# Kernel tuning notes

Hardware: AMD Instinct MI355X
Metric: run time of the kernel (lower is better)

Reference implementation:

```python
import jax, jax.numpy as jnp
import numpy as np

B, T, D = 2, 2048, 1024
H, HD = 16, 64
MAX_LEN = 2048


def setup_inputs() -> dict:
    key = jax.random.key(0)
    ks = jax.random.split(key, 7)
    s = 0.02
    return {
        "x": jax.random.normal(ks[0], (B, T, D), dtype=jnp.float32),
        "qkv_w": jax.random.normal(ks[1], (3 * D, D), dtype=jnp.float32) * s,
        "qkv_b": jax.random.normal(ks[2], (3 * D,), dtype=jnp.float32) * s,
        "out_w": jax.random.normal(ks[3], (D, D), dtype=jnp.float32) * s,
        "out_b": jax.random.normal(ks[4], (D,), dtype=jnp.float32) * s,
        "rel_pos": jax.random.normal(ks[5], (2 * MAX_LEN - 1, HD), dtype=jnp.float32),
        "rpe_w": jax.random.normal(ks[6], (HD,), dtype=jnp.float32) * s,
    }


def reference(x, qkv_w, qkv_b, out_w, out_b, rel_pos, rpe_w):
    Bq, Tq, Dq = x.shape
    scale = HD ** -0.5
    qkv = x @ qkv_w.T + qkv_b  # [B,T,3D]
    qkv = qkv.reshape(Bq, Tq, 3, H, HD)
    q = qkv[:, :, 0].transpose(0, 2, 1, 3)  # [B,H,T,HD]
    k = qkv[:, :, 1].transpose(0, 2, 1, 3)
    v = qkv[:, :, 2].transpose(0, 2, 1, 3)
    scores = jnp.einsum('bhqd,bhkd->bhqk', q, k) * scale  # [B,H,T,T]
    # relative position bias: gather rel embeddings, project to scalar
    rel_idx = jnp.arange(Tq)[None, :] - jnp.arange(Tq)[:, None] + MAX_LEN - 1  # [T,T]
    bias = (rel_pos @ rpe_w)[rel_idx]  # project first (cheap), then gather -> [T,T]
    scores = scores + bias[None, None]
    attn = jax.nn.softmax(scores, axis=-1)
    out = jnp.einsum('bhqk,bhkd->bhqd', attn, v)  # [B,H,T,HD]
    out = out.transpose(0, 2, 1, 3).reshape(Bq, Tq, Dq)
    return out @ out_w.T + out_b
```

## Files before the change

kernel.cpp:

```cpp
#include <hip/hip_runtime.h>
#include <math.h>

#define B_ 2
#define T_ 2048
#define D_ 1024
#define H_ 16
#define HD_ 64
#define MAXLEN_ 2048
#define N3D_ 3072
#define M_ (B_ * T_)
#define KA 1024

#define SCALE_L2E 0.18033688011116215f
#define L2E 1.4426950408889634f

typedef unsigned short ushort_t;
typedef __attribute__((ext_vector_type(8))) short short8;
typedef __attribute__((ext_vector_type(4))) float floatx4;
#define MFMA16(a, b, c) __builtin_amdgcn_mfma_f32_16x16x32_bf16(a, b, c, 0, 0, 0)

static __device__ __forceinline__ ushort_t f2bf(float f) {
    unsigned u = __float_as_uint(f);
    unsigned r = (u + 0x7FFFu + ((u >> 16) & 1u)) >> 16;
    return (ushort_t)r;
}
static __device__ __forceinline__ unsigned packrnu(float a, float b) {
    unsigned ua = __float_as_uint(a) + 0x8000u;
    unsigned ub = __float_as_uint(b) + 0x8000u;
    return __builtin_amdgcn_perm(ub, ua, 0x07060302u);
}

static __device__ __forceinline__ void gld16(const ushort_t* g, ushort_t* l) {
    __builtin_amdgcn_global_load_lds(
        (const __attribute__((address_space(1))) void*)g,
        (__attribute__((address_space(3))) void*)l, 16, 0, 0);
}

__global__ __launch_bounds__(256) void cvt_all(
    const float* __restrict__ x, const float* __restrict__ qw,
    const float* __restrict__ ow, const float* __restrict__ rel_pos,
    const float* __restrict__ rpe_w,
    ushort_t* __restrict__ Xc, ushort_t* __restrict__ QWc,
    ushort_t* __restrict__ OWc, float* __restrict__ biasp)
{
    const int row = blockIdx.x;
    if (row < M_ + N3D_ + D_) {
        const float* src; ushort_t* dst; int r;
        if (row < M_)            { src = x;  dst = Xc;  r = row; }
        else if (row < M_ + N3D_){ src = qw; dst = QWc; r = row - M_; }
        else                     { src = ow; dst = OWc; r = row - M_ - N3D_; }
        const int c = threadIdx.x * 4;
        float4 v = *(const float4*)(src + (size_t)r * 1024 + c);
        ushort4 hv;
        hv.x = f2bf(v.x); hv.y = f2bf(v.y); hv.z = f2bf(v.z); hv.w = f2bf(v.w);
        *(ushort4*)(dst + (size_t)r * KA + c) = hv;
    } else {
        const int wv = threadIdx.x >> 6, lane = threadIdx.x & 63;
        const int r = (row - (M_ + N3D_ + D_)) * 4 + wv;
        if (r < 2 * MAXLEN_ - 1) {
            float v = rel_pos[(size_t)r * HD_ + lane] * rpe_w[lane];
#pragma unroll
            for (int off = 32; off; off >>= 1) v += __shfl_down(v, off);
            if (lane == 0) biasp[r] = v * L2E;
        }
    }
}

__global__ __launch_bounds__(256) void qkv_mfma(
    const ushort_t* __restrict__ Ac, const ushort_t* __restrict__ Bc,
    const float* __restrict__ bias,
    ushort_t* __restrict__ Qs, ushort_t* __restrict__ Khi,
    ushort_t* __restrict__ Vt)
{
    __shared__ __align__(16) ushort_t As[2][16 * 512];
    __shared__ __align__(16) ushort_t Bs[2][16 * 512];
    const int tid = threadIdx.x;
    const int wv = tid >> 6, lane = tid & 63;
    const int l16 = lane & 15, quad = lane >> 4;
    const int wm = wv & 1, wn = wv >> 1;

    const int orig = blockIdx.y * 24 + blockIdx.x;
    const int swz = (orig & 7) * 96 + (orig >> 3);
    const int m0 = (swz / 24) * 128, n0 = (swz % 24) * 128;

    floatx4 acc[4][4];
#pragma unroll
    for (int i = 0; i < 4; ++i)
#pragma unroll
        for (int j = 0; j < 4; ++j) acc[i][j] = (floatx4){0.f, 0.f, 0.f, 0.f};

    auto stage = [&](int bufi, int kk) {
#pragma unroll
        for (int c = 0; c < 4; ++c) {
            const int b = wv * 4 + c;
            const int i = b >> 1, ks = b & 1;
            const int k = kk + ks * 32 + quad * 8;
            gld16(Ac + (size_t)(m0 + i * 16 + l16) * KA + k, As[bufi] + b * 512);
            gld16(Bc + (size_t)(n0 + i * 16 + l16) * KA + k, Bs[bufi] + b * 512);
        }
    };

    stage(0, 0);
    __syncthreads();

#pragma unroll 1
    for (int t = 0; t < 16; ++t) {
        const int cur = t & 1;
        if (t < 15) stage(cur ^ 1, (t + 1) * 64);
#pragma unroll
        for (int ks = 0; ks < 2; ++ks) {
            short8 af[4], bf[4];
#pragma unroll
            for (int ii = 0; ii < 4; ++ii)
                af[ii] = *(const short8*)(As[cur] + ((wm * 4 + ii) * 2 + ks) * 512 + lane * 8);
#pragma unroll
            for (int jj = 0; jj < 4; ++jj)
                bf[jj] = *(const short8*)(Bs[cur] + ((wn * 4 + jj) * 2 + ks) * 512 + lane * 8);
#pragma unroll
            for (int ii = 0; ii < 4; ++ii)
#pragma unroll
                for (int jj = 0; jj < 4; ++jj)
                    acc[ii][jj] = MFMA16(af[ii], bf[jj], acc[ii][jj]);
        }
        if (t < 15) __syncthreads();
    }

#pragma unroll
    for (int ii = 0; ii < 4; ++ii) {
#pragma unroll
        for (int r = 0; r < 4; ++r) {
            const int m = m0 + wm * 64 + ii * 16 + quad * 4 + r;
            const int bb = m >> 11, t = m & 2047;
#pragma unroll
            for (int jj = 0; jj < 4; ++jj) {
                const int n = n0 + wn * 64 + jj * 16 + l16;
                const int c = n >> 10, h = (n >> 6) & 15, hd = n & 63;
                const float v = acc[ii][jj][r] + bias[n];
                const size_t idx = (((size_t)bb * H_ + h) * T_ + t) * HD_ + hd;
                if (c == 0) { Qs[idx] = f2bf(v * SCALE_L2E); }
                else if (c == 1) { Khi[idx] = f2bf(v); }
                else { Vt[(((size_t)bb * H_ + h) * HD_ + hd) * T_ + t] = f2bf(v); }
            }
        }
    }
}

__global__ __launch_bounds__(256) void out_mfma(
    const ushort_t* __restrict__ Ac, const ushort_t* __restrict__ Bc,
    const float* __restrict__ bias, float* __restrict__ Out)
{
    __shared__ __align__(16) ushort_t As[2][16 * 512];
    __shared__ __align__(16) ushort_t Bs[2][8 * 512];
    const int tid = threadIdx.x;
    const int wv = tid >> 6, lane = tid & 63;
    const int l16 = lane & 15, quad = lane >> 4;
    const int wm = wv & 1, wn = wv >> 1;

    const int orig = blockIdx.y * 16 + blockIdx.x;
    const int swz = (orig & 7) * 64 + (orig >> 3);
    const int m0 = (swz >> 4) * 128, n0 = (swz & 15) * 64;

    floatx4 acc[4][2];
#pragma unroll
    for (int i = 0; i < 4; ++i)
#pragma unroll
        for (int j = 0; j < 2; ++j) acc[i][j] = (floatx4){0.f, 0.f, 0.f, 0.f};

    auto stage = [&](int bufi, int kk) {
#pragma unroll
        for (int c = 0; c < 4; ++c) {
            const int b = wv * 4 + c;
            const int i = b >> 1, ks = b & 1;
            const int k = kk + ks * 32 + quad * 8;
            gld16(Ac + (size_t)(m0 + i * 16 + l16) * KA + k, As[bufi] + b * 512);
        }
#pragma unroll
        for (int c = 0; c < 2; ++c) {
            const int b = wv * 2 + c;
            const int j = b >> 1, ks = b & 1;
            const int k = kk + ks * 32 + quad * 8;
            gld16(Bc + (size_t)(n0 + j * 16 + l16) * KA + k, Bs[bufi] + b * 512);
        }
    };

    stage(0, 0);
    __syncthreads();

#pragma unroll 1
    for (int t = 0; t < 16; ++t) {
        const int cur = t & 1;
        if (t < 15) stage(cur ^ 1, (t + 1) * 64);
#pragma unroll
        for (int ks = 0; ks < 2; ++ks) {
            short8 af[4], bf[2];
#pragma unroll
            for (int ii = 0; ii < 4; ++ii)
                af[ii] = *(const short8*)(As[cur] + ((wm * 4 + ii) * 2 + ks) * 512 + lane * 8);
#pragma unroll
            for (int jj = 0; jj < 2; ++jj)
                bf[jj] = *(const short8*)(Bs[cur] + ((wn * 2 + jj) * 2 + ks) * 512 + lane * 8);
#pragma unroll
            for (int ii = 0; ii < 4; ++ii)
#pragma unroll
                for (int jj = 0; jj < 2; ++jj)
                    acc[ii][jj] = MFMA16(af[ii], bf[jj], acc[ii][jj]);
        }
        if (t < 15) __syncthreads();
    }

#pragma unroll
    for (int ii = 0; ii < 4; ++ii) {
#pragma unroll
        for (int r = 0; r < 4; ++r) {
            const int m = m0 + wm * 64 + ii * 16 + quad * 4 + r;
#pragma unroll
            for (int jj = 0; jj < 2; ++jj) {
                const int n = n0 + wn * 32 + jj * 16 + l16;
                Out[(size_t)m * D_ + n] = acc[ii][jj][r] + bias[n];
            }
        }
    }
}

__global__ __launch_bounds__(256) void attn_mfma(
    const ushort_t* __restrict__ Qs, const ushort_t* __restrict__ Khi,
    const ushort_t* __restrict__ Vt, const float* __restrict__ biasp,
    ushort_t* __restrict__ AOc)
{
    __shared__ __align__(16) ushort_t KS[2][8 * 512];
    __shared__ __align__(16) ushort_t VS[2][8 * 512];
    __shared__ __align__(16) ushort_t PS[4][2][1024];

    const int i = blockIdx.x;
    const int j = i >> 3;
    const int bh = (i & 7) + 8 * (j >> 4);
    const int q0 = (j & 15) * 128;
    const int tid = threadIdx.x;
    const int wv = tid >> 6, lane = tid & 63;
    const int l16 = lane & 15, quad = lane >> 4;

    const int qw = q0 + wv * 32;

    short8 qh[2][2];
#pragma unroll
    for (int u = 0; u < 2; ++u) {
        const size_t qoff = ((size_t)bh * T_ + qw + u * 16 + l16) * HD_ + quad * 8;
        qh[u][0] = *(const short8*)(Qs + qoff);
        qh[u][1] = *(const short8*)(Qs + qoff + 32);
    }

    float l_r[2] = {0.f, 0.f};
    floatx4 o_acc[4][2];
#pragma unroll
    for (int g2 = 0; g2 < 4; ++g2)
#pragma unroll
        for (int u = 0; u < 2; ++u) o_acc[g2][u] = (floatx4){0.f, 0.f, 0.f, 0.f};

    const ushort_t* gK = Khi + (size_t)bh * T_ * HD_;
    const ushort_t* gV = Vt + (size_t)bh * HD_ * T_;
    const int c0base = 2047 + quad * 4 - (qw + 16 + l16);
    const int qdbase = quad >> 1;

    const size_t kstage = (size_t)(wv * 16 + l16) * HD_ + quad * 8;
    const size_t vstage = (size_t)(wv * 16 + l16) * T_ + quad * 8;

    gld16(gK + kstage,      KS[0] + (wv * 2 + 0) * 512);
    gld16(gK + kstage + 32, KS[0] + (wv * 2 + 1) * 512);
    gld16(gV + vstage,      VS[0] + (wv * 2 + 0) * 512);
    gld16(gV + vstage + 32, VS[0] + (wv * 2 + 1) * 512);
    __syncthreads();

    for (int t = 0; t < 32; ++t) {
        const int k0 = t * 64;
        const int buf = t & 1, nbuf = buf ^ 1;

        float4 f4[5];
        {
            const float* bp = biasp + (c0base + k0);
#pragma unroll
            for (int z = 0; z < 5; ++z)
                __builtin_memcpy(&f4[z], bp + z * 16, 16);
        }

        if (t < 31) {
            const size_t koff = kstage + (size_t)(k0 + 64) * HD_;
            gld16(gK + koff,      KS[nbuf] + (wv * 2 + 0) * 512);
            gld16(gK + koff + 32, KS[nbuf] + (wv * 2 + 1) * 512);
            const size_t voff = vstage + (size_t)(k0 + 64);
            gld16(gV + voff,      VS[nbuf] + (wv * 2 + 0) * 512);
            gld16(gV + voff + 32, VS[nbuf] + (wv * 2 + 1) * 512);
        }

#pragma unroll
        for (int g = 0; g < 4; ++g) {
            const short8 kh0 = *(const short8*)(KS[buf] + (g * 2 + 0) * 512 + lane * 8);
            const short8 kh1 = *(const short8*)(KS[buf] + (g * 2 + 1) * 512 + lane * 8);
            const int qd = 2 * (g & 1) + qdbase;
#pragma unroll
            for (int u = 0; u < 2; ++u) {
                const float4 bbv = f4[g + 1 - u];
                floatx4 a = (floatx4){bbv.x, bbv.y, bbv.z, bbv.w};
                a = MFMA16(kh0, qh[u][0], a);
                a = MFMA16(kh1, qh[u][1], a);
                const float p0 = __builtin_amdgcn_exp2f(a[0]);
                const float p1 = __builtin_amdgcn_exp2f(a[1]);
                const float p2 = __builtin_amdgcn_exp2f(a[2]);
                const float p3 = __builtin_amdgcn_exp2f(a[3]);
                l_r[u] += (p0 + p1) + (p2 + p3);
                uint2 pkd;
                pkd.x = packrnu(p0, p1);
                pkd.y = packrnu(p2, p3);
                *(uint2*)(PS[wv][u] + (g >> 1) * 512 + (qd * 16 + l16) * 8 + (quad & 1) * 4) = pkd;
            }
        }

        short8 pf[2][2];
#pragma unroll
        for (int u = 0; u < 2; ++u) {
            pf[u][0] = *(const short8*)(PS[wv][u] + lane * 8);
            pf[u][1] = *(const short8*)(PS[wv][u] + 512 + lane * 8);
        }

#pragma unroll
        for (int g2 = 0; g2 < 4; ++g2) {
            const short8 v0 = *(const short8*)(VS[buf] + (g2 * 2 + 0) * 512 + lane * 8);
            const short8 v1 = *(const short8*)(VS[buf] + (g2 * 2 + 1) * 512 + lane * 8);
#pragma unroll
            for (int u = 0; u < 2; ++u) {
                o_acc[g2][u] = MFMA16(v0, pf[u][0], o_acc[g2][u]);
                o_acc[g2][u] = MFMA16(v1, pf[u][1], o_acc[g2][u]);
            }
        }
        __syncthreads();
    }

    const int bb2 = bh >> 4, h2 = bh & 15;
#pragma unroll
    for (int u = 0; u < 2; ++u) {
        l_r[u] += __shfl_xor(l_r[u], 16);
        l_r[u] += __shfl_xor(l_r[u], 32);
        const float inv = 1.0f / l_r[u];
        const size_t m = (size_t)bb2 * T_ + qw + u * 16 + l16;
#pragma unroll
        for (int g2 = 0; g2 < 4; ++g2) {
            uint2 pk;
            pk.x = packrnu(o_acc[g2][u][0] * inv, o_acc[g2][u][1] * inv);
            pk.y = packrnu(o_acc[g2][u][2] * inv, o_acc[g2][u][3] * inv);
            *(uint2*)(AOc + m * KA + h2 * 64 + g2 * 16 + quad * 4) = pk;
        }
    }
}

extern "C" void kernel_launch(void* const* d_in, const int* in_sizes, int n_in,
                              void* d_out, int out_size, void* d_ws, size_t ws_size,
                              hipStream_t stream)
{
    const float* x       = (const float*)d_in[0];
    const float* qkv_w   = (const float*)d_in[1];
    const float* qkv_b   = (const float*)d_in[2];
    const float* out_w   = (const float*)d_in[3];
    const float* out_b   = (const float*)d_in[4];
    const float* rel_pos = (const float*)d_in[5];
    const float* rpe_w   = (const float*)d_in[6];
    float* out = (float*)d_out;

    const size_t QE = (size_t)B_ * H_ * T_ * HD_;
    ushort_t* Qs  = (ushort_t*)d_ws;
    ushort_t* Khi = Qs  + QE;
    ushort_t* Vt  = Khi + QE;
    ushort_t* Xc  = Vt  + QE;
    ushort_t* QWc = Xc  + (size_t)M_ * KA;
    ushort_t* OWc = QWc + (size_t)N3D_ * KA;
    ushort_t* AOc = OWc + (size_t)D_ * KA;
    float* biasp  = (float*)(AOc + (size_t)M_ * KA);

    cvt_all<<<M_ + N3D_ + D_ + 1024, 256, 0, stream>>>(
        x, qkv_w, out_w, rel_pos, rpe_w, Xc, QWc, OWc, biasp);

    qkv_mfma<<<dim3(N3D_ / 128, M_ / 128), 256, 0, stream>>>(
        Xc, QWc, qkv_b, Qs, Khi, Vt);
    attn_mfma<<<512, 256, 0, stream>>>(Qs, Khi, Vt, biasp, AOc);
    out_mfma<<<dim3(D_ / 64, M_ / 128), 256, 0, stream>>>(
        AOc, OWc, out_b, out);
}
```

Measured before the change: 257.9 us.

## Restructure QKV GEMM into 256x256 tiles with 8-wave ping-pong pipeline

Rewrites the QKV projection GEMM to use 512-thread blocks computing 256x256 output tiles, which cuts the grid from 768 to 192 blocks. Global loads are split into fine-grained stages and interleaved with MFMA quadrants, using explicit s_barrier, vmcnt waits and setprio to overlap loads with compute. Larger tiles raise data reuse per LDS byte, but the grid is now small relative to the CU count and register pressure is higher. The hand-coded barrier and waitcnt scheduling also carries a risk of ordering errors.

Result: faster. 241.9 us (-6.2%).

```diff
diff --git a/kernel.cpp b/kernel.cpp
--- a/kernel.cpp
+++ b/kernel.cpp
@@ -66,76 +66,111 @@
     }
 }
 
-__global__ __launch_bounds__(256) void qkv_mfma(
+__global__ __launch_bounds__(512, 2) void qkv_mfma(
     const ushort_t* __restrict__ Ac, const ushort_t* __restrict__ Bc,
     const float* __restrict__ bias,
     ushort_t* __restrict__ Qs, ushort_t* __restrict__ Khi,
     ushort_t* __restrict__ Vt)
 {
-    __shared__ __align__(16) ushort_t As[2][16 * 512];
-    __shared__ __align__(16) ushort_t Bs[2][16 * 512];
+    __shared__ __align__(16) ushort_t LDS[2][2][32 * 512];
+
     const int tid = threadIdx.x;
     const int wv = tid >> 6, lane = tid & 63;
     const int l16 = lane & 15, quad = lane >> 4;
-    const int wm = wv & 1, wn = wv >> 1;
-
-    const int orig = blockIdx.y * 24 + blockIdx.x;
-    const int swz = (orig & 7) * 96 + (orig >> 3);
-    const int m0 = (swz / 24) * 128, n0 = (swz % 24) * 128;
-
-    floatx4 acc[4][4];
-#pragma unroll
-    for (int i = 0; i < 4; ++i)
+    const int wr = wv >> 2, wc = wv & 3;
+
+    const int orig = blockIdx.y * 12 + blockIdx.x;
+    const int swz = (orig & 7) * 24 + (orig >> 3);
+    const int m0 = (swz / 12) * 256, n0 = (swz % 12) * 256;
+
+    floatx4 acc[8][4];
+#pragma unroll
+    for (int i = 0; i < 8; ++i)
 #pragma unroll
         for (int j = 0; j < 4; ++j) acc[i][j] = (floatx4){0.f, 0.f, 0.f, 0.f};
 
-    auto stage = [&](int bufi, int kk) {
-#pragma unroll
-        for (int c = 0; c < 4; ++c) {
-            const int b = wv * 4 + c;
-            const int i = b >> 1, ks = b & 1;
-            const int k = kk + ks * 32 + quad * 8;
-            gld16(Ac + (size_t)(m0 + i * 16 + l16) * KA + k, As[bufi] + b * 512);
-            gld16(Bc + (size_t)(n0 + i * 16 + l16) * KA + k, Bs[bufi] + b * 512);
-        }
-    };
-
-    stage(0, 0);
-    __syncthreads();
+    short8 af[4][2];
+    short8 bf[2][2][2];
+
+#define BARX() asm volatile("s_barrier" ::: "memory")
+#define WAITVM(n) asm volatile("s_waitcnt vmcnt(" #n ")" ::: "memory")
+
+#define STAGE(bufi, ab, unit, tile) do {                                      \
+    const ushort_t* _src = (ab) ? Bc : Ac;                                    \
+    const int _rc = (ab) ? n0 : m0;                                           \
+    const int _I = (unit) * 8 + wv;                                           \
+    const ushort_t* _g = _src + (size_t)(_rc + _I * 16 + l16) * KA            \
+                              + ((tile) * 64 + quad * 8);                     \
+    ushort_t* _l = &LDS[bufi][ab][(_I * 2) * 512];                            \
+    gld16(_g, _l);                                                            \
+    gld16(_g + 32, _l + 512);                                                 \
+} while (0)
+
+#define RD_AF(bufi, mi) do {                                                  \
+    _Pragma("unroll") for (int ii = 0; ii < 4; ++ii) {                        \
+        const int _I = wr * 8 + (mi) * 4 + ii;                                \
+        af[ii][0] = *(const short8*)(&LDS[bufi][0][(_I * 2 + 0) * 512] + lane * 8); \
+        af[ii][1] = *(const short8*)(&LDS[bufi][0][(_I * 2 + 1) * 512] + lane * 8); \
+    } } while (0)
+
+#define RD_BF(bufi, ni) do {                                                  \
+    _Pragma("unroll") for (int jj = 0; jj < 2; ++jj) {                        \
+        const int _I = wc * 4 + (ni) * 2 + jj;                                \
+        bf[ni][jj][0] = *(const short8*)(&LDS[bufi][1][(_I * 2 + 0) * 512] + lane * 8); \
+        bf[ni][jj][1] = *(const short8*)(&LDS[bufi][1][(_I * 2 + 1) * 512] + lane * 8); \
+    } } while (0)
+
+#define MM(mi, ni) do {                                                       \
+    __builtin_amdgcn_s_setprio(1);                                            \
+    _Pragma("unroll") for (int ii = 0; ii < 4; ++ii)                          \
+    _Pragma("unroll") for (int jj = 0; jj < 2; ++jj) {                        \
+        acc[(mi)*4+ii][(ni)*2+jj] = MFMA16(af[ii][0], bf[ni][jj][0], acc[(mi)*4+ii][(ni)*2+jj]); \
+        acc[(mi)*4+ii][(ni)*2+jj] = MFMA16(af[ii][1], bf[ni][jj][1], acc[(mi)*4+ii][(ni)*2+jj]); \
+    }                                                                         \
+    __builtin_amdgcn_s_setprio(0);                                            \
+} while (0)
+
+    STAGE(0, 1, 0, 0); STAGE(0, 1, 1, 0);
+    STAGE(0, 0, 0, 0); STAGE(0, 0, 1, 0);
+    STAGE(1, 1, 0, 1); STAGE(1, 1, 1, 1);
+    WAITVM(4);
+    BARX();
 
 #pragma unroll 1
-    for (int t = 0; t < 16; ++t) {
-        const int cur = t & 1;
-        if (t < 15) stage(cur ^ 1, (t + 1) * 64);
-#pragma unroll
-        for (int ks = 0; ks < 2; ++ks) {
-            short8 af[4], bf[4];
-#pragma unroll
-            for (int ii = 0; ii < 4; ++ii)
-                af[ii] = *(const short8*)(As[cur] + ((wm * 4 + ii) * 2 + ks) * 512 + lane * 8);
-#pragma unroll
-            for (int jj = 0; jj < 4; ++jj)
-                bf[jj] = *(const short8*)(Bs[cur] + ((wn * 4 + jj) * 2 + ks) * 512 + lane * 8);
-#pragma unroll
-            for (int ii = 0; ii < 4; ++ii)
-#pragma unroll
-                for (int jj = 0; jj < 4; ++jj)
-                    acc[ii][jj] = MFMA16(af[ii], bf[jj], acc[ii][jj]);
-        }
-        if (t < 15) __syncthreads();
-    }
-
-#pragma unroll
-    for (int ii = 0; ii < 4; ++ii) {
+    for (int j = 0; j < 8; ++j) {
+        const int tY  = 2 * j + 1;
+        const int tX2 = (2 * j + 2) & 15;
+        const int tY2 = (2 * j + 3) & 15;
+        RD_AF(0, 0); RD_BF(0, 0); STAGE(1, 0, 0, tY);  BARX(); MM(0, 0); BARX();
+        RD_BF(0, 1);              STAGE(1, 0, 1, tY);  BARX(); MM(0, 1); BARX();
+        RD_AF(0, 1);              STAGE(0, 1, 0, tX2); BARX(); MM(1, 0); BARX();
+                                  STAGE(0, 1, 1, tX2); BARX(); MM(1, 1);
+        WAITVM(4); BARX();
+        RD_AF(1, 0); RD_BF(1, 0); STAGE(0, 0, 0, tX2); BARX(); MM(0, 0); BARX();
+        RD_BF(1, 1);              STAGE(0, 0, 1, tX2); BARX(); MM(0, 1); BARX();
+        RD_AF(1, 1);              STAGE(1, 1, 0, tY2); BARX(); MM(1, 0); BARX();
+                                  STAGE(1, 1, 1, tY2); BARX(); MM(1, 1);
+        WAITVM(4); BARX();
+    }
+
+#undef BARX
+#undef WAITVM
+#undef STAGE
+#undef RD_AF
+#undef RD_BF
+#undef MM
+
+#pragma unroll
+    for (int mi = 0; mi < 8; ++mi) {
 #pragma unroll
         for (int r = 0; r < 4; ++r) {
-            const int m = m0 + wm * 64 + ii * 16 + quad * 4 + r;
+            const int m = m0 + wr * 128 + mi * 16 + quad * 4 + r;
             const int bb = m >> 11, t = m & 2047;
 #pragma unroll
             for (int jj = 0; jj < 4; ++jj) {
-                const int n = n0 + wn * 64 + jj * 16 + l16;
+                const int n = n0 + wc * 64 + jj * 16 + l16;
                 const int c = n >> 10, h = (n >> 6) & 15, hd = n & 63;
-                const float v = acc[ii][jj][r] + bias[n];
+                const float v = acc[mi][jj][r] + bias[n];
                 const size_t idx = (((size_t)bb * H_ + h) * T_ + t) * HD_ + hd;
                 if (c == 0) { Qs[idx] = f2bf(v * SCALE_L2E); }
                 else if (c == 1) { Khi[idx] = f2bf(v); }
@@ -377,7 +412,7 @@
     cvt_all<<<M_ + N3D_ + D_ + 1024, 256, 0, stream>>>(
         x, qkv_w, out_w, rel_pos, rpe_w, Xc, QWc, OWc, biasp);
 
-    qkv_mfma<<<dim3(N3D_ / 128, M_ / 128), 256, 0, stream>>>(
+    qkv_mfma<<<dim3(12, 16), 512, 0, stream>>>(
         Xc, QWc, qkv_b, Qs, Khi, Vt);
     attn_mfma<<<512, 256, 0, stream>>>(Qs, Khi, Vt, biasp, AOc);
     out_mfma<<<dim3(D_ / 64, M_ / 128), 256, 0, stream>>>(
```
